# Performance work log

Measured on AMD Instinct MI355X. Metric: run time of the kernel, lower is better.

## Reference

```python
import jax, jax.numpy as jnp
import numpy as np

DIM_INPUT = 1024
DIM_LATENT = 1024
DIM_HEAD = 64
INNER = max(DIM_INPUT, DIM_LATENT)  # 1024
HEADS = INNER // DIM_HEAD           # 16
SCALE = DIM_HEAD ** -0.5
RMS_EPS = 1e-8
LN_EPS = 1e-5


def layernorm(x, w, b):
    mu = jnp.mean(x, axis=-1, keepdims=True)
    var = jnp.var(x, axis=-1, keepdims=True)
    return (x - mu) * jax.lax.rsqrt(var + LN_EPS) * w + b


def rmsnorm(x, gamma):
    # x / clamp(||x||_2 * d^-0.5, eps) * gamma  (per-head, last dim = DIM_HEAD)
    norm = jnp.linalg.norm(x, axis=-1, keepdims=True) * (DIM_HEAD ** -0.5)
    return x / jnp.maximum(norm, RMS_EPS) * gamma


def setup_inputs() -> dict:
    key = jax.random.key(0)
    ks = jax.random.split(key, 10)
    b, n, m = 4, 2048, 256
    x = jax.random.normal(ks[0], (b, n, DIM_INPUT), dtype=jnp.float32)
    latents_c1 = jax.random.normal(ks[1], (b, m, DIM_LATENT), dtype=jnp.float32)
    latents_c0 = jax.random.normal(ks[2], (b, m, DIM_LATENT), dtype=jnp.float32)
    consciousness_mask = jax.random.randint(ks[3], (b, n), 0, 2).astype(bool)
    s = 0.02
    Wq = jax.random.normal(ks[4], (DIM_LATENT, INNER), dtype=jnp.float32) * s
    Wkv = jax.random.normal(ks[5], (DIM_INPUT, 2 * INNER), dtype=jnp.float32) * s
    Wout = jax.random.normal(ks[6], (INNER, DIM_LATENT), dtype=jnp.float32) * s
    bout = jnp.zeros((DIM_LATENT,), dtype=jnp.float32)
    ln_x_w = jnp.ones((DIM_INPUT,), dtype=jnp.float32)
    ln_x_b = jnp.zeros((DIM_INPUT,), dtype=jnp.float32)
    ln_l_w = jnp.ones((DIM_LATENT,), dtype=jnp.float32)
    ln_l_b = jnp.zeros((DIM_LATENT,), dtype=jnp.float32)
    gamma_q = jnp.ones((DIM_HEAD,), dtype=jnp.float32)
    gamma_k = jnp.ones((DIM_HEAD,), dtype=jnp.float32)
    return dict(x=x, latents_c1=latents_c1, latents_c0=latents_c0,
                consciousness_mask=consciousness_mask,
                ln_x_w=ln_x_w, ln_x_b=ln_x_b, ln_l_w=ln_l_w, ln_l_b=ln_l_b,
                gamma_q=gamma_q, gamma_k=gamma_k,
                Wq=Wq, Wkv=Wkv, Wout=Wout, bout=bout)


def reference(x, latents_c1, latents_c0, consciousness_mask,
              ln_x_w, ln_x_b, ln_l_w, ln_l_b, gamma_q, gamma_k,
              Wq, Wkv, Wout, bout):
    b, n, _ = x.shape
    m = latents_c1.shape[1]
    x = layernorm(x, ln_x_w, ln_x_b)
    l1 = layernorm(latents_c1, ln_l_w, ln_l_b)
    l0 = layernorm(latents_c0, ln_l_w, ln_l_b)

    # projections -> heads
    q1 = (l1 @ Wq).reshape(b, m, HEADS, DIM_HEAD).transpose(0, 2, 1, 3)  # b h m d
    q0 = (l0 @ Wq).reshape(b, m, HEADS, DIM_HEAD).transpose(0, 2, 1, 3)
    kv = x @ Wkv                                                         # b n 2*inner
    k, v = jnp.split(kv, 2, axis=-1)
    k = k.reshape(b, n, HEADS, DIM_HEAD).transpose(0, 2, 1, 3)           # b h n d
    v = v.reshape(b, n, HEADS, DIM_HEAD).transpose(0, 2, 1, 3)

    qn1 = rmsnorm(q1, gamma_q) * SCALE
    qn0 = rmsnorm(q0, gamma_q) * SCALE
    kn = rmsnorm(k, gamma_k)

    attn1 = jnp.einsum('bhid,bhjd->bhij', qn1, kn)
    attn0 = jnp.einsum('bhid,bhjd->bhij', qn0, kn)

    neg = -jnp.finfo(attn1.dtype).max
    attn1 = jnp.where(consciousness_mask[:, None, None, :], attn1, neg)
    # NOTE: source only masks the c1 stream; c0 is left unmasked (faithful).

    attn1 = jax.nn.softmax(attn1, axis=-1)
    attn0 = jax.nn.softmax(attn0, axis=-1)

    o1 = jnp.einsum('bhij,bhjd->bhid', attn1, v).transpose(0, 2, 1, 3).reshape(b, m, INNER)
    o0 = jnp.einsum('bhij,bhjd->bhid', attn0, v).transpose(0, 2, 1, 3).reshape(b, m, INNER)
    return (o1 @ Wout + bout, o0 @ Wout + bout)
```

## Files before the change

kernel.cpp:

```cpp
#include <hip/hip_runtime.h>
#include <hip/hip_bf16.h>
#include <float.h>
#include <math.h>

#define BB 4
#define NN 2048
#define MM 256
#define DIN 1024
#define INNER 1024
#define NHEADS 16
#define DHEAD 64

typedef __attribute__((ext_vector_type(8))) short bf16x8;
typedef __attribute__((ext_vector_type(4))) float f32x4;
typedef __attribute__((ext_vector_type(4))) unsigned int u32x4;

__device__ __forceinline__ unsigned short f2bf(float f) {
    unsigned int u = __builtin_bit_cast(unsigned int, f);
    u = (u + 0x7fffu + ((u >> 16) & 1u)) >> 16;
    return (unsigned short)u;
}

__device__ __forceinline__ float fexp2(float x) {
#if __has_builtin(__builtin_amdgcn_exp2f)
    return __builtin_amdgcn_exp2f(x);
#else
    float r; asm("v_exp_f32 %0, %1" : "=v"(r) : "v"(x)); return r;
#endif
}

__device__ __forceinline__ unsigned int cvt_pk_bf16(float a, float b) {
    unsigned int r;
    asm("v_cvt_pk_bf16_f32 %0, %1, %2" : "=v"(r) : "v"(a), "v"(b));
    return r;
}

__device__ __forceinline__ void gload_lds16(const void* g, void* l) {
    __builtin_amdgcn_global_load_lds((__attribute__((address_space(1))) void*)(g),
                                     (__attribute__((address_space(3))) void*)(l),
                                     16, 0, 0);
}

#define LOG2E 1.4426950408889634f

__device__ __forceinline__ void ln_row(const float* __restrict__ srow,
                                       unsigned short* __restrict__ drow,
                                       const float* __restrict__ w,
                                       const float* __restrict__ bv) {
    const int tid = threadIdx.x;
    const float4 v = ((const float4*)srow)[tid];
    float sum = v.x + v.y + v.z + v.w;
    float sq  = v.x * v.x + v.y * v.y + v.z * v.z + v.w * v.w;
    #pragma unroll
    for (int off = 32; off; off >>= 1) {
        sum += __shfl_down(sum, off);
        sq  += __shfl_down(sq, off);
    }
    __shared__ float ls[4], lq[4];
    const int wv = tid >> 6;
    if ((tid & 63) == 0) { ls[wv] = sum; lq[wv] = sq; }
    __syncthreads();
    sum = ls[0] + ls[1] + ls[2] + ls[3];
    sq  = lq[0] + lq[1] + lq[2] + lq[3];
    const float mu  = sum * (1.0f / 1024.0f);
    const float var = sq * (1.0f / 1024.0f) - mu * mu;
    const float rs  = rsqrtf(var + 1e-5f);
    const float4 w4 = ((const float4*)w)[tid];
    const float4 b4 = ((const float4*)bv)[tid];
    ushort4 o;
    o.x = f2bf((v.x - mu) * rs * w4.x + b4.x);
    o.y = f2bf((v.y - mu) * rs * w4.y + b4.y);
    o.z = f2bf((v.z - mu) * rs * w4.z + b4.z);
    o.w = f2bf((v.w - mu) * rs * w4.w + b4.w);
    ((ushort4*)drow)[tid] = o;
}

__global__ __launch_bounds__(256) void ln_bf16_kernel(const float* __restrict__ src,
                                                      unsigned short* __restrict__ dst,
                                                      const float* __restrict__ w,
                                                      const float* __restrict__ bv) {
    const int row = blockIdx.x;
    ln_row(src + (size_t)row * 1024, dst + (size_t)row * 1024, w, bv);
}

__global__ __launch_bounds__(256) void ln2_bf16_kernel(const float* __restrict__ src1,
                                                       const float* __restrict__ src2,
                                                       int split,
                                                       unsigned short* __restrict__ dst,
                                                       const float* __restrict__ w,
                                                       const float* __restrict__ bv) {
    const int row = blockIdx.x;
    const float* s = (row < split) ? (src1 + (size_t)row * 1024)
                                   : (src2 + (size_t)(row - split) * 1024);
    ln_row(s, dst + (size_t)row * 1024, w, bv);
}

__global__ __launch_bounds__(256) void transpose_cast_kernel(const float* __restrict__ W,
                                                             unsigned short* __restrict__ WT,
                                                             int K, int N) {
    __shared__ float t[32][33];
    const int k0 = blockIdx.y * 32, n0 = blockIdx.x * 32;
    const int tx = threadIdx.x & 31, ty8 = threadIdx.x >> 5;
    #pragma unroll
    for (int i = 0; i < 4; i++) {
        const int k = ty8 + i * 8;
        t[k][tx] = W[(size_t)(k0 + k) * N + n0 + tx];
    }
    __syncthreads();
    #pragma unroll
    for (int i = 0; i < 4; i++) {
        const int n = ty8 + i * 8;
        WT[(size_t)(n0 + n) * K + k0 + tx] = f2bf(t[tx][n]);
    }
}

__global__ __launch_bounds__(256) void v_transpose_bf16(const unsigned short* __restrict__ vbh,
                                                        unsigned short* __restrict__ vth) {
    __shared__ unsigned short t[32][34];
    const int n0 = blockIdx.x * 32;
    const int d0 = blockIdx.y * 32;
    const int bh = blockIdx.z;
    const int b = bh >> 4, h = bh & 15;
    const int tx = threadIdx.x & 31, ty8 = threadIdx.x >> 5;
    #pragma unroll
    for (int i = 0; i < 4; i++) {
        const int nr = ty8 + i * 8;
        t[nr][tx] = vbh[(size_t)(b * NN + n0 + nr) * 1024 + h * 64 + d0 + tx];
    }
    __syncthreads();
    #pragma unroll
    for (int i = 0; i < 4; i++) {
        const int dr = ty8 + i * 8;
        vth[((size_t)(b * 16 + h) * 64 + d0 + dr) * 2048 + n0 + tx] = t[tx][dr];
    }
}

#define GEMM_STAGE(AS, BS, kt)                                                        \
    {                                                                                 \
        _Pragma("unroll")                                                             \
        for (int e = 0; e < EA; e++) {                                                \
            const int r0 = (w * EA + e) * 16;                                         \
            gload_lds16(Ag + (size_t)(r0 + srow) * K + (kt) + selt, &AS[r0 * 32]);    \
        }                                                                             \
        _Pragma("unroll")                                                             \
        for (int e = 0; e < 2; e++) {                                                 \
            const int r0 = (w * 2 + e) * 16;                                          \
            gload_lds16(Bg + (size_t)(r0 + srow) * K + (kt) + selt, &BS[r0 * 32]);    \
        }                                                                             \
    }

#define GEMM_COMPUTE(AS, BS)                                                          \
    {                                                                                 \
        bf16x8 af[MREP], bfv[4];                                                      \
        _Pragma("unroll")                                                             \
        for (int m = 0; m < MREP; m++)                                                \
            af[m] = *(const bf16x8*)&AS[(wr * (BM / 2) + m * 16 + (l & 15)) * 32 + (l >> 4) * 8]; \
        _Pragma("unroll")                                                             \
        for (int n = 0; n < 4; n++)                                                   \
            bfv[n] = *(const bf16x8*)&BS[(wc * 64 + n * 16 + (l & 15)) * 32 + (l >> 4) * 8]; \
        _Pragma("unroll")                                                             \
        for (int m = 0; m < MREP; m++)                                                \
            _Pragma("unroll")                                                         \
            for (int n = 0; n < 4; n++)                                               \
                acc[m][n] = __builtin_amdgcn_mfma_f32_16x16x32_bf16(af[m], bfv[n], acc[m][n], 0, 0, 0); \
    }

template<int MODE, int BM>
__global__ __launch_bounds__(256) void gemm_bf16_kernel(const unsigned short* __restrict__ A,
                                                        const unsigned short* __restrict__ BT,
                                                        float* __restrict__ C,
                                                        unsigned short* __restrict__ outK,
                                                        unsigned short* __restrict__ outV,
                                                        int M, int N, int K,
                                                        const float* __restrict__ aux) {
    constexpr int MREP = BM / 32;
    constexpr int EA = BM / 64;
    __shared__ __align__(16) unsigned short As0[BM * 32];
    __shared__ __align__(16) unsigned short As1[BM * 32];
    __shared__ __align__(16) unsigned short Bs0[128 * 32];
    __shared__ __align__(16) unsigned short Bs1[128 * 32];
    const int tid = threadIdx.x;
    const int l = tid & 63, w = tid >> 6;
    const int wr = w >> 1, wc = w & 1;

    const int gx = gridDim.x;
    const int flat = blockIdx.y * gx + blockIdx.x;
    const int cpx = (gx * gridDim.y) >> 3;
    const int swz = (flat & 7) * cpx + (flat >> 3);
    const int rb = (swz / gx) * BM, cb = (swz % gx) * 128;

    f32x4 acc[MREP][4];
    #pragma unroll
    for (int m = 0; m < MREP; m++)
        #pragma unroll
        for (int n = 0; n < 4; n++) acc[m][n] = (f32x4){0.0f, 0.0f, 0.0f, 0.0f};

    const int srow = l >> 2;
    const int selt = (l & 3) * 8;
    const unsigned short* Ag = A + (size_t)rb * K;
    const unsigned short* Bg = BT + (size_t)cb * K;

    GEMM_STAGE(As0, Bs0, 0);
    __syncthreads();
    int kt = 0;
    for (; kt + 64 < K; kt += 64) {
        GEMM_STAGE(As1, Bs1, kt + 32);
        GEMM_COMPUTE(As0, Bs0);
        __syncthreads();
        GEMM_STAGE(As0, Bs0, kt + 64);
        GEMM_COMPUTE(As1, Bs1);
        __syncthreads();
    }
    GEMM_STAGE(As1, Bs1, kt + 32);
    GEMM_COMPUTE(As0, Bs0);
    __syncthreads();
    GEMM_COMPUTE(As1, Bs1);

    const int lx = l & 15;
    const int col0 = cb + wc * 64;
    const int row0 = rb + wr * (BM / 2) + (l >> 4) * 4;

    if constexpr (MODE == 0) {
        #pragma unroll
        for (int m = 0; m < MREP; m++) {
            #pragma unroll
            for (int n = 0; n < 4; n++) {
                const int col = col0 + n * 16 + lx;
                const float badd = aux[col];
                #pragma unroll
                for (int r = 0; r < 4; r++)
                    C[(size_t)(row0 + m * 16 + r) * N + col] = acc[m][n][r] + badd;
            }
        }
    } else {
        const bool isK = (MODE == 2) || (col0 < (N >> 1));
        if (isK) {
            float g4[4];
            #pragma unroll
            for (int n = 0; n < 4; n++) g4[n] = aux[n * 16 + lx];
            const float fin = (MODE == 2) ? (0.125f * LOG2E) : 1.0f;
            #pragma unroll
            for (int m = 0; m < MREP; m++) {
                #pragma unroll
                for (int r = 0; r < 4; r++) {
                    float ss = 0.0f;
                    #pragma unroll
                    for (int n = 0; n < 4; n++) ss += acc[m][n][r] * acc[m][n][r];
                    ss += __shfl_xor(ss, 1);
                    ss += __shfl_xor(ss, 2);
                    ss += __shfl_xor(ss, 4);
                    ss += __shfl_xor(ss, 8);
                    const float inv = fin / fmaxf(sqrtf(ss) * 0.125f, 1e-8f);
                    const size_t rbase = (size_t)(row0 + m * 16 + r) * 1024 + col0;
                    #pragma unroll
                    for (int n = 0; n < 4; n++)
                        outK[rbase + n * 16 + lx] = f2bf(acc[m][n][r] * inv * g4[n]);
                }
            }
        } else {
            const int colv = col0 - 1024;
            #pragma unroll
            for (int m = 0; m < MREP; m++) {
                #pragma unroll
                for (int r = 0; r < 4; r++) {
                    const size_t rbase = (size_t)(row0 + m * 16 + r) * 1024 + colv;
                    #pragma unroll
                    for (int n = 0; n < 4; n++)
                        outV[rbase + n * 16 + lx] = f2bf(acc[m][n][r]);
                }
            }
        }
    }
}

__global__ __launch_bounds__(256) void attn_mfma_kernel(const unsigned short* __restrict__ qbh,
                                                        const unsigned short* __restrict__ kbh,
                                                        const unsigned short* __restrict__ vth,
                                                        const int* __restrict__ mask,
                                                        unsigned short* __restrict__ obuf) {
    const int bh = blockIdx.x;
    const int qt = blockIdx.y;
    const int sid = blockIdx.z;
    const int b = bh >> 4, h = bh & 15;
    const int tid = threadIdx.x;
    const int l = tid & 63, w = tid >> 6;
    const int lq = l & 15, g = l >> 4;

    __shared__ __align__(16) unsigned short KVs[2][8192];
    __shared__ int Ms[2][64];

    bf16x8 aq[2];
    const size_t qrow = (size_t)((sid * BB + b) * MM + qt * 64 + w * 16 + lq);
    #pragma unroll
    for (int ks = 0; ks < 2; ks++)
        aq[ks] = *(const bf16x8*)&qbh[qrow * 1024 + h * 64 + ks * 32 + g * 8];

    const int srow0 = tid >> 3, srow1 = (tid >> 3) + 32, sc8 = tid & 7;
    const unsigned short* kgb = kbh + (size_t)(b * NN) * 1024 + h * 64;
    const unsigned short* vgb = vth + ((size_t)(b * 16 + h) * 64) * 2048;
    bf16x8 kreg0, kreg1, vreg0, vreg1;
    int mreg = 0;

#define ATT_LOAD(t0)                                                                  \
    {                                                                                 \
        kreg0 = *(const bf16x8*)&kgb[(size_t)((t0) + srow0) * 1024 + sc8 * 8];        \
        kreg1 = *(const bf16x8*)&kgb[(size_t)((t0) + srow1) * 1024 + sc8 * 8];        \
        vreg0 = *(const bf16x8*)&vgb[(size_t)srow0 * 2048 + (t0) + sc8 * 8];          \
        vreg1 = *(const bf16x8*)&vgb[(size_t)srow1 * 2048 + (t0) + sc8 * 8];          \
        if (tid < 64) mreg = mask[b * NN + (t0) + tid];                               \
    }

#define ATT_WRITE(buf)                                                                \
    {                                                                                 \
        unsigned short* kd = &KVs[buf][0];                                            \
        *(bf16x8*)&kd[srow0 * 64 + ((sc8 ^ (srow0 & 7)) * 8)] = kreg0;                \
        *(bf16x8*)&kd[srow1 * 64 + ((sc8 ^ (srow1 & 7)) * 8)] = kreg1;                \
        unsigned short* vd = &KVs[buf][4096];                                         \
        *(bf16x8*)&vd[srow0 * 64 + ((sc8 ^ (srow0 & 7)) * 8)] = vreg0;                \
        *(bf16x8*)&vd[srow1 * 64 + ((sc8 ^ (srow1 & 7)) * 8)] = vreg1;                \
        if (tid < 64) Ms[buf][tid] = mreg;                                            \
    }

    f32x4 oacc[4];
    #pragma unroll
    for (int n = 0; n < 4; n++) oacc[n] = (f32x4){0.0f, 0.0f, 0.0f, 0.0f};
    float mrun = -FLT_MAX, lrun = 0.0f;

    ATT_LOAD(0);
    ATT_WRITE(0);
    __syncthreads();
    int cur = 0;

    for (int t0 = 0; t0 < NN; t0 += 64) {
        const bool nxt = (t0 + 64 < NN);
        if (nxt) ATT_LOAD(t0 + 64);

        const unsigned short* kcur = &KVs[cur][0];
        const unsigned short* vcur = &KVs[cur][4096];

        f32x4 st[4];
        #pragma unroll
        for (int j = 0; j < 4; j++) st[j] = (f32x4){0.0f, 0.0f, 0.0f, 0.0f};
        #pragma unroll
        for (int j = 0; j < 4; j++) {
            #pragma unroll
            for (int ks = 0; ks < 2; ks++) {
                const int row = j * 16 + lq;
                const bf16x8 kf = *(const bf16x8*)&kcur[row * 64 + (((ks * 4 + g) ^ (row & 7)) * 8)];
                st[j] = __builtin_amdgcn_mfma_f32_16x16x32_bf16(kf, aq[ks], st[j], 0, 0, 0);
            }
        }

        float p[4][4];
        #pragma unroll
        for (int j = 0; j < 4; j++) {
            if (sid == 0) {
                const int4 mj = *(const int4*)&Ms[cur][j * 16 + g * 4];
                p[j][0] = mj.x ? st[j][0] : -3.0e38f;
                p[j][1] = mj.y ? st[j][1] : -3.0e38f;
                p[j][2] = mj.z ? st[j][2] : -3.0e38f;
                p[j][3] = mj.w ? st[j][3] : -3.0e38f;
            } else {
                #pragma unroll
                for (int r = 0; r < 4; r++) p[j][r] = st[j][r];
            }
        }

        float mloc = fmaxf(fmaxf(p[0][0], p[0][1]), fmaxf(p[0][2], p[0][3]));
        #pragma unroll
        for (int j = 1; j < 4; j++)
            mloc = fmaxf(mloc, fmaxf(fmaxf(p[j][0], p[j][1]), fmaxf(p[j][2], p[j][3])));
        mloc = fmaxf(mloc, __shfl_xor(mloc, 16));
        mloc = fmaxf(mloc, __shfl_xor(mloc, 32));

        if (__any(mloc > mrun + 8.0f)) {
            const float mn = fmaxf(mrun, mloc);
            const float scal = fexp2(mrun - mn);
            mrun = mn;
            lrun *= scal;
            float oscal[4];
            #pragma unroll
            for (int r = 0; r < 4; r++) oscal[r] = __shfl(scal, g * 4 + r);
            #pragma unroll
            for (int n = 0; n < 4; n++)
                #pragma unroll
                for (int r = 0; r < 4; r++) oacc[n][r] *= oscal[r];
        }

        float rsum = 0.0f;
        #pragma unroll
        for (int j = 0; j < 4; j++)
            #pragma unroll
            for (int r = 0; r < 4; r++) { p[j][r] = fexp2(p[j][r] - mrun); rsum += p[j][r]; }
        rsum += __shfl_xor(rsum, 16);
        rsum += __shfl_xor(rsum, 32);
        lrun += rsum;

        unsigned int packed[4][2];
        #pragma unroll
        for (int jt = 0; jt < 4; jt++)
            #pragma unroll
            for (int hh = 0; hh < 2; hh++)
                packed[jt][hh] = cvt_pk_bf16(p[jt][2 * hh], p[jt][2 * hh + 1]);

        #pragma unroll
        for (int ks = 0; ks < 2; ks++) {
            unsigned int wds[4];
            #pragma unroll
            for (int wd = 0; wd < 4; wd++) {
                const int src = lq + 16 * ((g & 1) * 2 + (wd >> 1));
                const unsigned int vA = (unsigned int)__shfl((int)packed[ks * 2][wd & 1], src);
                const unsigned int vB = (unsigned int)__shfl((int)packed[ks * 2 + 1][wd & 1], src);
                wds[wd] = (g & 2) ? vB : vA;
            }
            const u32x4 tmp = {wds[0], wds[1], wds[2], wds[3]};
            const bf16x8 afP = __builtin_bit_cast(bf16x8, tmp);
            #pragma unroll
            for (int n = 0; n < 4; n++) {
                const int drow = n * 16 + lq;
                const bf16x8 bv = *(const bf16x8*)&vcur[drow * 64 + (((ks * 4 + g) ^ (drow & 7)) * 8)];
                oacc[n] = __builtin_amdgcn_mfma_f32_16x16x32_bf16(afP, bv, oacc[n], 0, 0, 0);
            }
        }

        if (nxt) {
            ATT_WRITE(cur ^ 1);
            __syncthreads();
        }
        cur ^= 1;
    }

    const float il = 1.0f / lrun;
    float linv[4];
    #pragma unroll
    for (int r = 0; r < 4; r++) linv[r] = __shfl(il, g * 4 + r);
    unsigned short* ob = obuf + ((size_t)((sid * BB + b) * MM + qt * 64 + w * 16)) * 1024 + h * 64;
    #pragma unroll
    for (int n = 0; n < 4; n++)
        #pragma unroll
        for (int r = 0; r < 4; r++)
            ob[(size_t)(g * 4 + r) * 1024 + n * 16 + lq] = f2bf(oacc[n][r] * linv[r]);
}

extern "C" void kernel_launch(void* const* d_in, const int* in_sizes, int n_in,
                              void* d_out, int out_size, void* d_ws, size_t ws_size,
                              hipStream_t stream) {
    const float* x      = (const float*)d_in[0];
    const float* lc1    = (const float*)d_in[1];
    const float* lc0    = (const float*)d_in[2];
    const int*   mask   = (const int*)d_in[3];
    const float* ln_x_w = (const float*)d_in[4];
    const float* ln_x_b = (const float*)d_in[5];
    const float* ln_l_w = (const float*)d_in[6];
    const float* ln_l_b = (const float*)d_in[7];
    const float* g_q    = (const float*)d_in[8];
    const float* g_k    = (const float*)d_in[9];
    const float* Wq     = (const float*)d_in[10];
    const float* Wkv    = (const float*)d_in[11];
    const float* Wout   = (const float*)d_in[12];
    const float* bout   = (const float*)d_in[13];
    float* out = (float*)d_out;

    char* p = (char*)d_ws;
    unsigned short* xnb   = (unsigned short*)p; p += (size_t)8388608 * 2;
    unsigned short* latb  = (unsigned short*)p; p += (size_t)2097152 * 2;
    unsigned short* obb   = (unsigned short*)p; p += (size_t)2097152 * 2;
    unsigned short* WkvT  = (unsigned short*)p; p += (size_t)2097152 * 2;
    unsigned short* WqT   = (unsigned short*)p; p += (size_t)1048576 * 2;
    unsigned short* WoutT = (unsigned short*)p; p += (size_t)1048576 * 2;
    unsigned short* qbh   = (unsigned short*)p; p += (size_t)2097152 * 2;
    unsigned short* kbh   = (unsigned short*)p; p += (size_t)8388608 * 2;
    unsigned short* vbh   = (unsigned short*)p; p += (size_t)8388608 * 2;
    unsigned short* vth   = (unsigned short*)p; p += (size_t)8388608 * 2;

    ln_bf16_kernel<<<BB * NN, 256, 0, stream>>>(x, xnb, ln_x_w, ln_x_b);
    ln2_bf16_kernel<<<2 * BB * MM, 256, 0, stream>>>(lc1, lc0, BB * MM, latb, ln_l_w, ln_l_b);

    transpose_cast_kernel<<<dim3(2048 / 32, 1024 / 32), 256, 0, stream>>>(Wkv, WkvT, 1024, 2048);
    transpose_cast_kernel<<<dim3(1024 / 32, 1024 / 32), 256, 0, stream>>>(Wq, WqT, 1024, 1024);
    transpose_cast_kernel<<<dim3(1024 / 32, 1024 / 32), 256, 0, stream>>>(Wout, WoutT, 1024, 1024);

    gemm_bf16_kernel<1, 128><<<dim3(2048 / 128, 8192 / 128), 256, 0, stream>>>(
        xnb, WkvT, nullptr, kbh, vbh, 8192, 2048, 1024, g_k);
    gemm_bf16_kernel<2, 64><<<dim3(1024 / 128, 2048 / 64), 256, 0, stream>>>(
        latb, WqT, nullptr, qbh, nullptr, 2048, 1024, 1024, g_q);

    v_transpose_bf16<<<dim3(NN / 32, 2, BB * NHEADS), 256, 0, stream>>>(vbh, vth);

    attn_mfma_kernel<<<dim3(BB * NHEADS, MM / 64, 2), 256, 0, stream>>>(qbh, kbh, vth, mask, obb);

    gemm_bf16_kernel<0, 64><<<dim3(1024 / 128, 2048 / 64), 256, 0, stream>>>(
        obb, WoutT, out, nullptr, nullptr, 2048, 1024, 1024, bout);
}
```

Baseline: 256.5 us.

## Triple-buffer GEMM LDS pipeline and merge layernorm and transpose launches

The GEMM moves from double-buffered LDS staging to a three-stage ring buffer. Explicit vmcnt waits and a single barrier per k-tile replace the paired __syncthreads, so global-to-LDS loads can run two tiles ahead of the MFMA compute. The two layernorm kernels are merged into one launch, and the three weight transpose-casts are merged into one launch using a z-dimension selector with early exit. This cuts launch overhead and exposed load latency, at the cost of more LDS per block (which may lower occupancy) and hand-tuned waitcnt counts that must match the number of issued loads.

Result: slower. 295.5 us (+15.2%).

```diff
diff --git a/kernel.cpp b/kernel.cpp
--- a/kernel.cpp
+++ b/kernel.cpp
@@ -43,10 +43,29 @@
 
 #define LOG2E 1.4426950408889634f
 
-__device__ __forceinline__ void ln_row(const float* __restrict__ srow,
-                                       unsigned short* __restrict__ drow,
-                                       const float* __restrict__ w,
-                                       const float* __restrict__ bv) {
+__global__ __launch_bounds__(256) void ln_all_kernel(const float* __restrict__ x,
+                                                     const float* __restrict__ lc1,
+                                                     const float* __restrict__ lc0,
+                                                     unsigned short* __restrict__ xnb,
+                                                     unsigned short* __restrict__ latb,
+                                                     const float* __restrict__ xw,
+                                                     const float* __restrict__ xb,
+                                                     const float* __restrict__ lw,
+                                                     const float* __restrict__ lb) {
+    const int row = blockIdx.x;
+    const float* srow;
+    unsigned short* drow;
+    const float *w, *bv;
+    if (row < BB * NN) {
+        srow = x + (size_t)row * 1024; drow = xnb + (size_t)row * 1024;
+        w = xw; bv = xb;
+    } else {
+        const int r2 = row - BB * NN;
+        srow = (r2 < BB * MM) ? (lc1 + (size_t)r2 * 1024)
+                              : (lc0 + (size_t)(r2 - BB * MM) * 1024);
+        drow = latb + (size_t)r2 * 1024;
+        w = lw; bv = lb;
+    }
     const int tid = threadIdx.x;
     const float4 v = ((const float4*)srow)[tid];
     float sum = v.x + v.y + v.z + v.w;
@@ -75,29 +94,21 @@
     ((ushort4*)drow)[tid] = o;
 }
 
-__global__ __launch_bounds__(256) void ln_bf16_kernel(const float* __restrict__ src,
-                                                      unsigned short* __restrict__ dst,
-                                                      const float* __restrict__ w,
-                                                      const float* __restrict__ bv) {
-    const int row = blockIdx.x;
-    ln_row(src + (size_t)row * 1024, dst + (size_t)row * 1024, w, bv);
-}
-
-__global__ __launch_bounds__(256) void ln2_bf16_kernel(const float* __restrict__ src1,
-                                                       const float* __restrict__ src2,
-                                                       int split,
-                                                       unsigned short* __restrict__ dst,
-                                                       const float* __restrict__ w,
-                                                       const float* __restrict__ bv) {
-    const int row = blockIdx.x;
-    const float* s = (row < split) ? (src1 + (size_t)row * 1024)
-                                   : (src2 + (size_t)(row - split) * 1024);
-    ln_row(s, dst + (size_t)row * 1024, w, bv);
-}
-
-__global__ __launch_bounds__(256) void transpose_cast_kernel(const float* __restrict__ W,
-                                                             unsigned short* __restrict__ WT,
-                                                             int K, int N) {
+__global__ __launch_bounds__(256) void transpose_all_kernel(const float* __restrict__ Wkv,
+                                                            const float* __restrict__ Wq,
+                                                            const float* __restrict__ Wout,
+                                                            unsigned short* __restrict__ WkvT,
+                                                            unsigned short* __restrict__ WqT,
+                                                            unsigned short* __restrict__ WoutT) {
+    const int z = blockIdx.z;
+    const float* W;
+    unsigned short* WT;
+    int N;
+    if (z == 0)      { W = Wkv;  WT = WkvT;  N = 2048; }
+    else if (z == 1) { W = Wq;   WT = WqT;   N = 1024; }
+    else             { W = Wout; WT = WoutT; N = 1024; }
+    if (blockIdx.x * 32 >= N) return;
+    const int K = 1024;
     __shared__ float t[32][33];
     const int k0 = blockIdx.y * 32, n0 = blockIdx.x * 32;
     const int tx = threadIdx.x & 31, ty8 = threadIdx.x >> 5;
@@ -135,35 +146,45 @@
     }
 }
 
-#define GEMM_STAGE(AS, BS, kt)                                                        \
+#define GEMM_STAGE(buf, ktile)                                                        \
     {                                                                                 \
+        unsigned short* Ab = &As[buf][0];                                             \
+        unsigned short* Bb = &Bs[buf][0];                                             \
         _Pragma("unroll")                                                             \
         for (int e = 0; e < EA; e++) {                                                \
             const int r0 = (w * EA + e) * 16;                                         \
-            gload_lds16(Ag + (size_t)(r0 + srow) * K + (kt) + selt, &AS[r0 * 32]);    \
+            gload_lds16(Ag + (size_t)(r0 + srow) * K + (ktile) * 32 + selt, &Ab[r0 * 32]); \
         }                                                                             \
         _Pragma("unroll")                                                             \
         for (int e = 0; e < 2; e++) {                                                 \
             const int r0 = (w * 2 + e) * 16;                                          \
-            gload_lds16(Bg + (size_t)(r0 + srow) * K + (kt) + selt, &BS[r0 * 32]);    \
+            gload_lds16(Bg + (size_t)(r0 + srow) * K + (ktile) * 32 + selt, &Bb[r0 * 32]); \
         }                                                                             \
     }
 
-#define GEMM_COMPUTE(AS, BS)                                                          \
+#define GEMM_COMPUTE(buf)                                                             \
     {                                                                                 \
+        const unsigned short* Ab = &As[buf][0];                                       \
+        const unsigned short* Bb = &Bs[buf][0];                                       \
         bf16x8 af[MREP], bfv[4];                                                      \
         _Pragma("unroll")                                                             \
         for (int m = 0; m < MREP; m++)                                                \
-            af[m] = *(const bf16x8*)&AS[(wr * (BM / 2) + m * 16 + (l & 15)) * 32 + (l >> 4) * 8]; \
+            af[m] = *(const bf16x8*)&Ab[(wr * (BM / 2) + m * 16 + (l & 15)) * 32 + (l >> 4) * 8]; \
         _Pragma("unroll")                                                             \
         for (int n = 0; n < 4; n++)                                                   \
-            bfv[n] = *(const bf16x8*)&BS[(wc * 64 + n * 16 + (l & 15)) * 32 + (l >> 4) * 8]; \
+            bfv[n] = *(const bf16x8*)&Bb[(wc * 64 + n * 16 + (l & 15)) * 32 + (l >> 4) * 8]; \
         _Pragma("unroll")                                                             \
         for (int m = 0; m < MREP; m++)                                                \
             _Pragma("unroll")                                                         \
             for (int n = 0; n < 4; n++)                                               \
                 acc[m][n] = __builtin_amdgcn_mfma_f32_16x16x32_bf16(af[m], bfv[n], acc[m][n], 0, 0, 0); \
     }
+
+#define VM_LPS                                                                        \
+    { if constexpr (BM == 128) asm volatile("s_waitcnt vmcnt(4)" ::: "memory");       \
+      else                     asm volatile("s_waitcnt vmcnt(3)" ::: "memory"); }
+#define VM_ZERO  asm volatile("s_waitcnt vmcnt(0)" ::: "memory");
+#define BARRIER  __builtin_amdgcn_s_barrier();
 
 template<int MODE, int BM>
 __global__ __launch_bounds__(256) void gemm_bf16_kernel(const unsigned short* __restrict__ A,
@@ -175,10 +196,8 @@
                                                         const float* __restrict__ aux) {
     constexpr int MREP = BM / 32;
     constexpr int EA = BM / 64;
-    __shared__ __align__(16) unsigned short As0[BM * 32];
-    __shared__ __align__(16) unsigned short As1[BM * 32];
-    __shared__ __align__(16) unsigned short Bs0[128 * 32];
-    __shared__ __align__(16) unsigned short Bs1[128 * 32];
+    __shared__ __align__(16) unsigned short As[3][BM * 32];
+    __shared__ __align__(16) unsigned short Bs[3][128 * 32];
     const int tid = threadIdx.x;
     const int l = tid & 63, w = tid >> 6;
     const int wr = w >> 1, wc = w & 1;
@@ -200,21 +219,24 @@
     const unsigned short* Ag = A + (size_t)rb * K;
     const unsigned short* Bg = BT + (size_t)cb * K;
 
-    GEMM_STAGE(As0, Bs0, 0);
-    __syncthreads();
-    int kt = 0;
-    for (; kt + 64 < K; kt += 64) {
-        GEMM_STAGE(As1, Bs1, kt + 32);
-        GEMM_COMPUTE(As0, Bs0);
-        __syncthreads();
-        GEMM_STAGE(As0, Bs0, kt + 64);
-        GEMM_COMPUTE(As1, Bs1);
-        __syncthreads();
-    }
-    GEMM_STAGE(As1, Bs1, kt + 32);
-    GEMM_COMPUTE(As0, Bs0);
-    __syncthreads();
-    GEMM_COMPUTE(As1, Bs1);
+    const int nt = K >> 5;
+    GEMM_STAGE(0, 0);
+    GEMM_STAGE(1, 1);
+    VM_LPS;
+    BARRIER;
+    for (int i = 0; i < nt; i++) {
+        const int bi = i - (i / 3) * 3;
+        if (i + 2 < nt) {
+            const int bs = (i + 2) - ((i + 2) / 3) * 3;
+            GEMM_STAGE(bs, i + 2);
+            GEMM_COMPUTE(bi);
+            VM_LPS;
+        } else {
+            GEMM_COMPUTE(bi);
+            VM_ZERO;
+        }
+        BARRIER;
+    }
 
     const int lx = l & 15;
     const int col0 = cb + wc * 64;
@@ -473,12 +495,11 @@
     unsigned short* vbh   = (unsigned short*)p; p += (size_t)8388608 * 2;
     unsigned short* vth   = (unsigned short*)p; p += (size_t)8388608 * 2;
 
-    ln_bf16_kernel<<<BB * NN, 256, 0, stream>>>(x, xnb, ln_x_w, ln_x_b);
-    ln2_bf16_kernel<<<2 * BB * MM, 256, 0, stream>>>(lc1, lc0, BB * MM, latb, ln_l_w, ln_l_b);
-
-    transpose_cast_kernel<<<dim3(2048 / 32, 1024 / 32), 256, 0, stream>>>(Wkv, WkvT, 1024, 2048);
-    transpose_cast_kernel<<<dim3(1024 / 32, 1024 / 32), 256, 0, stream>>>(Wq, WqT, 1024, 1024);
-    transpose_cast_kernel<<<dim3(1024 / 32, 1024 / 32), 256, 0, stream>>>(Wout, WoutT, 1024, 1024);
+    ln_all_kernel<<<BB * NN + 2 * BB * MM, 256, 0, stream>>>(
+        x, lc1, lc0, xnb, latb, ln_x_w, ln_x_b, ln_l_w, ln_l_b);
+
+    transpose_all_kernel<<<dim3(64, 32, 3), 256, 0, stream>>>(
+        Wkv, Wq, Wout, WkvT, WqT, WoutT);
 
     gemm_bf16_kernel<1, 128><<<dim3(2048 / 128, 8192 / 128), 256, 0, stream>>>(
         xnb, WkvT, nullptr, kbh, vbh, 8192, 2048, 1024, g_k);
```
